# Optimization experiments

Hardware: AMD Instinct MI355X
Metric: run time of the kernel (lower is better)

Reference implementation:

```python
import jax, jax.numpy as jnp
import numpy as np

D_MODEL = 1024
NUM_HEADS = 16
HEAD_DIM = D_MODEL // NUM_HEADS
BATCH, SEQ = 4, 4096


def setup_inputs() -> dict:
    key = jax.random.key(0)
    ks = jax.random.split(key, 12)
    std = 0.02
    inp = {
        "query": jax.random.normal(ks[0], (BATCH, SEQ, D_MODEL), dtype=jnp.float32),
        "key": jax.random.normal(ks[1], (BATCH, SEQ, D_MODEL), dtype=jnp.float32),
        "value": jax.random.normal(ks[2], (BATCH, SEQ, D_MODEL), dtype=jnp.float32),
        "mask": jax.random.randint(ks[3], (BATCH, SEQ, 1, 1), 0, 2, dtype=jnp.int32),
        "Wq": jax.random.normal(ks[4], (D_MODEL, D_MODEL), dtype=jnp.float32) * std,
        "bq": jnp.zeros((D_MODEL,), dtype=jnp.float32),
        "Wk": jax.random.normal(ks[5], (D_MODEL, D_MODEL), dtype=jnp.float32) * std,
        "bk": jnp.zeros((D_MODEL,), dtype=jnp.float32),
        "Wv": jax.random.normal(ks[6], (D_MODEL, D_MODEL), dtype=jnp.float32) * std,
        "bv": jnp.zeros((D_MODEL,), dtype=jnp.float32),
        "Wo": jax.random.normal(ks[7], (D_MODEL, D_MODEL), dtype=jnp.float32) * std,
        "bo": jnp.zeros((D_MODEL,), dtype=jnp.float32),
    }
    return inp


def reference(query, key, value, mask, Wq, bq, Wk, bk, Wv, bv, Wo, bo):
    b = query.shape[0]
    # QKV projections (torch nn.Linear: x @ W.T + b)
    Q = query @ Wq.T + bq
    K = key @ Wk.T + bk
    V = value @ Wv.T + bv
    # [b, s, H, hd] -> [b, H, s, hd]
    Q = Q.reshape(b, -1, NUM_HEADS, HEAD_DIM).transpose(0, 2, 1, 3)
    K = K.reshape(b, -1, NUM_HEADS, HEAD_DIM).transpose(0, 2, 1, 3)
    V = V.reshape(b, -1, NUM_HEADS, HEAD_DIM).transpose(0, 2, 1, 3)
    # NOTE: faithful to the original's mislabeled einsum: tensors are [b,H,s,hd]
    # but labels treat axis1 as 'q' and axis2 as 'h', so energy is
    # [batch, seq, heads_q, heads_k] and softmax mixes over heads.
    energy = jnp.einsum('nqhd,nkhd->nhqk', Q, K)
    energy = jnp.where(mask == 0, jnp.float32(-1e20), energy)
    attention = jax.nn.softmax(energy / jnp.sqrt(jnp.float32(D_MODEL)), axis=3)
    # output labeled nqhd -> [b, heads, seq, hd]
    x = jnp.einsum('nhql,nlhd->nqhd', attention, V)
    x = x.transpose(0, 2, 1, 3).reshape(b, -1, D_MODEL)  # [b, s, d_model]
    return x @ Wo.T + bo
```

## Files before the change

kernel.cpp:

```cpp
#include <hip/hip_runtime.h>


typedef unsigned int u32;
typedef unsigned short u16;
typedef __attribute__((ext_vector_type(4))) float f32x4;
typedef __attribute__((ext_vector_type(8))) short bf16x8;

__device__ __forceinline__ void async_copy16(const void* g, void* l) {
  __builtin_amdgcn_global_load_lds(
      (const __attribute__((address_space(1))) void*)g,
      (__attribute__((address_space(3))) void*)l, 16, 0, 0);
}

__device__ __forceinline__ u32 pk_bf16(float a, float b) {
  u32 ua = (__builtin_bit_cast(u32, a) + 0x8000u) >> 16;
  u32 ub = (__builtin_bit_cast(u32, b) + 0x8000u) & 0xFFFF0000u;
  return ua | ub;
}
__device__ __forceinline__ float bflo(u32 u) { return __builtin_bit_cast(float, u << 16); }
__device__ __forceinline__ float bfhi(u32 u) { return __builtin_bit_cast(float, u & 0xFFFF0000u); }

struct F8 { float f[8]; };
__device__ __forceinline__ F8 unp8(uint4 u) {
  F8 r;
  r.f[0] = bflo(u.x); r.f[1] = bfhi(u.x);
  r.f[2] = bflo(u.y); r.f[3] = bfhi(u.y);
  r.f[4] = bflo(u.z); r.f[5] = bfhi(u.z);
  r.f[6] = bflo(u.w); r.f[7] = bfhi(u.w);
  return r;
}

__global__ void cvt_w4(const float* __restrict__ s0, const float* __restrict__ s1,
                       const float* __restrict__ s2, const float* __restrict__ s3,
                       u16* __restrict__ dst) {
  int z = blockIdx.y;
  const float* s = (z == 0) ? s0 : (z == 1) ? s1 : (z == 2) ? s2 : s3;
  u16* d = dst + (size_t)z * (1024 * 1024);
  int i = (blockIdx.x * 256 + threadIdx.x) * 4;
  float4 f = *(const float4*)(s + i);
  uint2 u;
  u.x = pk_bf16(f.x, f.y);
  u.y = pk_bf16(f.z, f.w);
  *(uint2*)(d + i) = u;
}

template <bool AF32, bool OUTBF>
__device__ __forceinline__ void gemm_tile(const void* __restrict__ Ap,
                                          const u16* __restrict__ Bp,
                                          const float* __restrict__ bias,
                                          void* __restrict__ Cp,
                                          int m0, int n0, u16* As, u16* Bs) {
  constexpr int KD = 1024;
  constexpr int ND = 1024;
  const int t = threadIdx.x;
  const int lane = t & 63, w = t >> 6;
  const int wr = (w >> 1) * 64, wc = (w & 1) * 64;
  const int lr = lane & 15, quad = lane >> 4;
  f32x4 acc[4][4] = {};

  for (int k0 = 0; k0 < KD; k0 += 32) {
    __syncthreads();
#pragma unroll
    for (int i = 0; i < 2; i++) {
      int c = i * 256 + t;
      int r = c >> 2, c8 = (c & 3) * 8;
      async_copy16(Bp + ((size_t)(n0 + r) * KD + k0 + c8), &Bs[c * 8]);
    }
    if constexpr (AF32) {
      const float* Af = (const float*)Ap;
      const int r = t >> 2, c8 = (t & 3) * 8;
      const float4* s0 = (const float4*)(Af + (size_t)(m0 + r) * KD + k0 + c8);
      const float4* s1 = (const float4*)(Af + (size_t)(m0 + 64 + r) * KD + k0 + c8);
      float4 f0 = s0[0], f1 = s0[1];
      float4 f2 = s1[0], f3 = s1[1];
      uint4 u0 = { pk_bf16(f0.x, f0.y), pk_bf16(f0.z, f0.w),
                   pk_bf16(f1.x, f1.y), pk_bf16(f1.z, f1.w) };
      uint4 u1 = { pk_bf16(f2.x, f2.y), pk_bf16(f2.z, f2.w),
                   pk_bf16(f3.x, f3.y), pk_bf16(f3.z, f3.w) };
      *(uint4*)&As[t * 8] = u0;
      *(uint4*)&As[(256 + t) * 8] = u1;
    } else {
      const u16* Ab = (const u16*)Ap;
#pragma unroll
      for (int i = 0; i < 2; i++) {
        int c = i * 256 + t;
        int r = c >> 2, c8 = (c & 3) * 8;
        async_copy16(Ab + ((size_t)(m0 + r) * KD + k0 + c8), &As[c * 8]);
      }
    }
    __syncthreads();

    bf16x8 af[4], bfr[4];
#pragma unroll
    for (int mi = 0; mi < 4; mi++)
      af[mi] = *(const bf16x8*)&As[(wr + mi * 16 + lr) * 32 + quad * 8];
#pragma unroll
    for (int ni = 0; ni < 4; ni++)
      bfr[ni] = *(const bf16x8*)&Bs[(wc + ni * 16 + lr) * 32 + quad * 8];
#pragma unroll
    for (int mi = 0; mi < 4; mi++)
#pragma unroll
      for (int ni = 0; ni < 4; ni++)
        acc[mi][ni] = __builtin_amdgcn_mfma_f32_16x16x32_bf16(af[mi], bfr[ni], acc[mi][ni], 0, 0, 0);
  }

#pragma unroll
  for (int ni = 0; ni < 4; ni++) {
    int col = n0 + wc + ni * 16 + lr;
    float bv = bias[col];
#pragma unroll
    for (int mi = 0; mi < 4; mi++) {
      int row = m0 + wr + mi * 16 + quad * 4;
#pragma unroll
      for (int r = 0; r < 4; r++) {
        float val = acc[mi][ni][r] + bv;
        if constexpr (OUTBF) {
          ((u16*)Cp)[(size_t)(row + r) * ND + col] =
              (u16)((__builtin_bit_cast(u32, val) + 0x8000u) >> 16);
        } else {
          ((float*)Cp)[(size_t)(row + r) * ND + col] = val;
        }
      }
    }
  }
}

__global__ __launch_bounds__(256) void gemm_qkv(
    const float* __restrict__ q, const float* __restrict__ k, const float* __restrict__ v,
    const u16* __restrict__ W, const float* __restrict__ bq, const float* __restrict__ bk,
    const float* __restrict__ bv, u16* __restrict__ out) {
  __shared__ alignas(16) u16 As[128 * 32];
  __shared__ alignas(16) u16 Bs[128 * 32];
  const int z = blockIdx.z;
  const float* A = (z == 0) ? q : (z == 1) ? k : v;
  const float* bias = (z == 0) ? bq : (z == 1) ? bk : bv;
  gemm_tile<true, true>(A, W + (size_t)z * 1048576, bias, out + (size_t)z * 16777216,
                        blockIdx.x * 128, blockIdx.y * 128, As, Bs);
}

__global__ __launch_bounds__(256) void gemm_o(
    const u16* __restrict__ X, const u16* __restrict__ W,
    const float* __restrict__ bias, float* __restrict__ C) {
  __shared__ alignas(16) u16 As[128 * 32];
  __shared__ alignas(16) u16 Bs[128 * 32];
  gemm_tile<false, false>(X, W, bias, C, blockIdx.x * 128, blockIdx.y * 128, As, Bs);
}

__global__ __launch_bounds__(256) void attn_mix(
    const u16* __restrict__ Q, const u16* __restrict__ K,
    const u16* __restrict__ V, const int* __restrict__ mask,
    u16* __restrict__ X) {
  __shared__ alignas(16) u16 qs[4][1024];
  __shared__ alignas(16) u16 ks[4][1024];
  __shared__ alignas(16) u16 vs[4][1024];

  const int w = threadIdx.x >> 6;
  const int lane = threadIdx.x & 63;
  const int p = blockIdx.x * 4 + w;
  const size_t base = (size_t)p * 1024;

  {
    const uint4* Qg = (const uint4*)(Q + base);
    const uint4* Kg = (const uint4*)(K + base);
    const uint4* Vg = (const uint4*)(V + base);
    uint4* ql = (uint4*)qs[w]; uint4* kl = (uint4*)ks[w]; uint4* vl = (uint4*)vs[w];
    ql[lane] = Qg[lane]; ql[64 + lane] = Qg[64 + lane];
    kl[lane] = Kg[lane]; kl[64 + lane] = Kg[64 + lane];
    vl[lane] = Vg[lane]; vl[64 + lane] = Vg[64 + lane];
  }
  const int mk = mask[p];

  const int qh = lane >> 2, g = lane & 3;
  float e0 = 0.f, e1 = 0.f, e2 = 0.f, e3 = 0.f;
  {
    const uint4* qr = (const uint4*)&qs[w][qh * 64];
    const uint4* k0r = (const uint4*)&ks[w][(g * 4 + 0) * 64];
    const uint4* k1r = (const uint4*)&ks[w][(g * 4 + 1) * 64];
    const uint4* k2r = (const uint4*)&ks[w][(g * 4 + 2) * 64];
    const uint4* k3r = (const uint4*)&ks[w][(g * 4 + 3) * 64];
#pragma unroll
    for (int c = 0; c < 8; c++) {
      F8 qf = unp8(qr[c]);
      F8 ka = unp8(k0r[c]), kb = unp8(k1r[c]), kc = unp8(k2r[c]), kd = unp8(k3r[c]);
#pragma unroll
      for (int j = 0; j < 8; j++) {
        e0 += qf.f[j] * ka.f[j];
        e1 += qf.f[j] * kb.f[j];
        e2 += qf.f[j] * kc.f[j];
        e3 += qf.f[j] * kd.f[j];
      }
    }
  }
  const float sc = mk ? 0.03125f : 0.0f;
  float v0 = e0 * sc, v1 = e1 * sc, v2 = e2 * sc, v3 = e3 * sc;
  float mx = fmaxf(fmaxf(v0, v1), fmaxf(v2, v3));
  mx = fmaxf(mx, __shfl_xor(mx, 1, 64));
  mx = fmaxf(mx, __shfl_xor(mx, 2, 64));
  float p0 = __expf(v0 - mx), p1 = __expf(v1 - mx), p2 = __expf(v2 - mx), p3 = __expf(v3 - mx);
  float s = p0 + p1 + p2 + p3;
  s += __shfl_xor(s, 1, 64);
  s += __shfl_xor(s, 2, 64);
  float inv = 1.0f / s;
  float a0 = p0 * inv, a1 = p1 * inv, a2 = p2 * inv, a3 = p3 * inv;

  const int c4 = g;
  float xa[16];
#pragma unroll
  for (int i = 0; i < 16; i++) xa[i] = 0.f;
#pragma unroll
  for (int g2 = 0; g2 < 4; g2++) {
    int src = (lane & ~3) | g2;
    float w0 = __shfl(a0, src, 64);
    float w1 = __shfl(a1, src, 64);
    float w2 = __shfl(a2, src, 64);
    float w3 = __shfl(a3, src, 64);
    const float wv[4] = { w0, w1, w2, w3 };
#pragma unroll
    for (int j4 = 0; j4 < 4; j4++) {
      int kh = g2 * 4 + j4;
      float wgt = wv[j4];
      F8 va = unp8(*(const uint4*)&vs[w][kh * 64 + c4 * 16]);
      F8 vb = unp8(*(const uint4*)&vs[w][kh * 64 + c4 * 16 + 8]);
#pragma unroll
      for (int j = 0; j < 8; j++) {
        xa[j] += wgt * va.f[j];
        xa[8 + j] += wgt * vb.f[j];
      }
    }
  }
  uint4 o0 = { pk_bf16(xa[0], xa[1]), pk_bf16(xa[2], xa[3]),
               pk_bf16(xa[4], xa[5]), pk_bf16(xa[6], xa[7]) };
  uint4 o1 = { pk_bf16(xa[8], xa[9]), pk_bf16(xa[10], xa[11]),
               pk_bf16(xa[12], xa[13]), pk_bf16(xa[14], xa[15]) };
  uint4* Xp = (uint4*)(X + base);
  Xp[lane * 2] = o0;
  Xp[lane * 2 + 1] = o1;
}

extern "C" void kernel_launch(void* const* d_in, const int* in_sizes, int n_in,
                              void* d_out, int out_size, void* d_ws, size_t ws_size,
                              hipStream_t stream) {
  const float* q    = (const float*)d_in[0];
  const float* k    = (const float*)d_in[1];
  const float* v    = (const float*)d_in[2];
  const int*   mask = (const int*)d_in[3];
  const float* Wq   = (const float*)d_in[4];
  const float* bq   = (const float*)d_in[5];
  const float* Wk   = (const float*)d_in[6];
  const float* bk   = (const float*)d_in[7];
  const float* Wv   = (const float*)d_in[8];
  const float* bv   = (const float*)d_in[9];
  const float* Wo   = (const float*)d_in[10];
  const float* bo   = (const float*)d_in[11];

  u16* wsb = (u16*)d_ws;
  u16* Wqkv = wsb;
  u16* Wob  = wsb + 3145728;
  u16* Qb   = wsb + 4194304;
  u16* Kb   = Qb + 16777216;
  u16* Vb   = Kb + 16777216;
  u16* Xb   = Vb + 16777216;

  cvt_w4<<<dim3(1024, 4), 256, 0, stream>>>(Wq, Wk, Wv, Wo, wsb);
  gemm_qkv<<<dim3(128, 8, 3), 256, 0, stream>>>(q, k, v, Wqkv, bq, bk, bv, Qb);
  attn_mix<<<4096, 256, 0, stream>>>(Qb, Kb, Vb, mask, Xb);
  gemm_o<<<dim3(128, 8), 256, 0, stream>>>(Xb, Wob, bo, (float*)d_out);
}
```

Before: 483.4 us.

## Pre-convert QKV inputs to bf16, remap GEMM tile order, pad attention LDS rows

When the workspace is large enough, a new kernel converts the fp32 query/key/value activations to bf16 before the QKV GEMM, so the GEMM streams half the bytes and skips per-tile conversion. The cost is an extra full pass over the inputs. Both GEMMs now use a linearized grid with a remapped block order that groups tiles sharing A rows, aiming at better L2 reuse. The attention kernel pads each 64-element head row in shared memory to 72 elements to reduce LDS bank conflicts.

```diff
diff --git a/kernel.cpp b/kernel.cpp
--- a/kernel.cpp
+++ b/kernel.cpp
@@ -36,6 +36,19 @@
   int z = blockIdx.y;
   const float* s = (z == 0) ? s0 : (z == 1) ? s1 : (z == 2) ? s2 : s3;
   u16* d = dst + (size_t)z * (1024 * 1024);
+  int i = (blockIdx.x * 256 + threadIdx.x) * 4;
+  float4 f = *(const float4*)(s + i);
+  uint2 u;
+  u.x = pk_bf16(f.x, f.y);
+  u.y = pk_bf16(f.z, f.w);
+  *(uint2*)(d + i) = u;
+}
+
+__global__ void cvt_in3(const float* __restrict__ s0, const float* __restrict__ s1,
+                        const float* __restrict__ s2, u16* __restrict__ dst) {
+  int z = blockIdx.y;
+  const float* s = (z == 0) ? s0 : (z == 1) ? s1 : s2;
+  u16* d = dst + (size_t)z * 16777216;
   int i = (blockIdx.x * 256 + threadIdx.x) * 4;
   float4 f = *(const float4*)(s + i);
   uint2 u;
@@ -125,17 +138,24 @@
   }
 }
 
+template <bool AF32>
 __global__ __launch_bounds__(256) void gemm_qkv(
-    const float* __restrict__ q, const float* __restrict__ k, const float* __restrict__ v,
-    const u16* __restrict__ W, const float* __restrict__ bq, const float* __restrict__ bk,
-    const float* __restrict__ bv, u16* __restrict__ out) {
+    const void* __restrict__ a0, const void* __restrict__ a1, const void* __restrict__ a2,
+    const u16* __restrict__ W, const float* __restrict__ b0, const float* __restrict__ b1,
+    const float* __restrict__ b2, u16* __restrict__ out) {
   __shared__ alignas(16) u16 As[128 * 32];
   __shared__ alignas(16) u16 Bs[128 * 32];
-  const int z = blockIdx.z;
-  const float* A = (z == 0) ? q : (z == 1) ? k : v;
-  const float* bias = (z == 0) ? bq : (z == 1) ? bk : bv;
-  gemm_tile<true, true>(A, W + (size_t)z * 1048576, bias, out + (size_t)z * 16777216,
-                        blockIdx.x * 128, blockIdx.y * 128, As, Bs);
+  const int lin = blockIdx.x;
+  const int c = lin & 7;
+  const int i = lin >> 3;
+  const int z = i >> 7;
+  const int r = i & 127;
+  const int m = c * 16 + (r >> 3);
+  const int n = r & 7;
+  const void* A = (z == 0) ? a0 : (z == 1) ? a1 : a2;
+  const float* bias = (z == 0) ? b0 : (z == 1) ? b1 : b2;
+  gemm_tile<AF32, true>(A, W + (size_t)z * 1048576, bias, out + (size_t)z * 16777216,
+                        m * 128, n * 128, As, Bs);
 }
 
 __global__ __launch_bounds__(256) void gemm_o(
@@ -143,16 +163,22 @@
     const float* __restrict__ bias, float* __restrict__ C) {
   __shared__ alignas(16) u16 As[128 * 32];
   __shared__ alignas(16) u16 Bs[128 * 32];
-  gemm_tile<false, false>(X, W, bias, C, blockIdx.x * 128, blockIdx.y * 128, As, Bs);
+  const int lin = blockIdx.x;
+  const int c = lin & 7;
+  const int i = lin >> 3;
+  const int m = c * 16 + (i >> 3);
+  const int n = i & 7;
+  gemm_tile<false, false>(X, W, bias, C, m * 128, n * 128, As, Bs);
 }
 
 __global__ __launch_bounds__(256) void attn_mix(
     const u16* __restrict__ Q, const u16* __restrict__ K,
     const u16* __restrict__ V, const int* __restrict__ mask,
     u16* __restrict__ X) {
-  __shared__ alignas(16) u16 qs[4][1024];
-  __shared__ alignas(16) u16 ks[4][1024];
-  __shared__ alignas(16) u16 vs[4][1024];
+  constexpr int RS = 72;
+  __shared__ alignas(16) u16 qs[4][16 * RS];
+  __shared__ alignas(16) u16 ks[4][16 * RS];
+  __shared__ alignas(16) u16 vs[4][16 * RS];
 
   const int w = threadIdx.x >> 6;
   const int lane = threadIdx.x & 63;
@@ -163,25 +189,32 @@
     const uint4* Qg = (const uint4*)(Q + base);
     const uint4* Kg = (const uint4*)(K + base);
     const uint4* Vg = (const uint4*)(V + base);
-    uint4* ql = (uint4*)qs[w]; uint4* kl = (uint4*)ks[w]; uint4* vl = (uint4*)vs[w];
-    ql[lane] = Qg[lane]; ql[64 + lane] = Qg[64 + lane];
-    kl[lane] = Kg[lane]; kl[64 + lane] = Kg[64 + lane];
-    vl[lane] = Vg[lane]; vl[64 + lane] = Vg[64 + lane];
+#pragma unroll
+    for (int h = 0; h < 2; h++) {
+      int j = h * 64 + lane;
+      int off = (j >> 3) * RS + (j & 7) * 8;
+      *(uint4*)&qs[w][off] = Qg[j];
+      *(uint4*)&ks[w][off] = Kg[j];
+      *(uint4*)&vs[w][off] = Vg[j];
+    }
   }
   const int mk = mask[p];
 
   const int qh = lane >> 2, g = lane & 3;
   float e0 = 0.f, e1 = 0.f, e2 = 0.f, e3 = 0.f;
   {
-    const uint4* qr = (const uint4*)&qs[w][qh * 64];
-    const uint4* k0r = (const uint4*)&ks[w][(g * 4 + 0) * 64];
-    const uint4* k1r = (const uint4*)&ks[w][(g * 4 + 1) * 64];
-    const uint4* k2r = (const uint4*)&ks[w][(g * 4 + 2) * 64];
-    const uint4* k3r = (const uint4*)&ks[w][(g * 4 + 3) * 64];
+    const u16* qr = &qs[w][qh * RS];
+    const u16* k0r = &ks[w][(g * 4 + 0) * RS];
+    const u16* k1r = &ks[w][(g * 4 + 1) * RS];
+    const u16* k2r = &ks[w][(g * 4 + 2) * RS];
+    const u16* k3r = &ks[w][(g * 4 + 3) * RS];
 #pragma unroll
     for (int c = 0; c < 8; c++) {
-      F8 qf = unp8(qr[c]);
-      F8 ka = unp8(k0r[c]), kb = unp8(k1r[c]), kc = unp8(k2r[c]), kd = unp8(k3r[c]);
+      F8 qf = unp8(*(const uint4*)&qr[c * 8]);
+      F8 ka = unp8(*(const uint4*)&k0r[c * 8]);
+      F8 kb = unp8(*(const uint4*)&k1r[c * 8]);
+      F8 kc = unp8(*(const uint4*)&k2r[c * 8]);
+      F8 kd = unp8(*(const uint4*)&k3r[c * 8]);
 #pragma unroll
       for (int j = 0; j < 8; j++) {
         e0 += qf.f[j] * ka.f[j];
@@ -203,7 +236,6 @@
   float inv = 1.0f / s;
   float a0 = p0 * inv, a1 = p1 * inv, a2 = p2 * inv, a3 = p3 * inv;
 
-  const int c4 = g;
   float xa[16];
 #pragma unroll
   for (int i = 0; i < 16; i++) xa[i] = 0.f;
@@ -219,8 +251,8 @@
     for (int j4 = 0; j4 < 4; j4++) {
       int kh = g2 * 4 + j4;
       float wgt = wv[j4];
-      F8 va = unp8(*(const uint4*)&vs[w][kh * 64 + c4 * 16]);
-      F8 vb = unp8(*(const uint4*)&vs[w][kh * 64 + c4 * 16 + 8]);
+      F8 va = unp8(*(const uint4*)&vs[w][kh * RS + g * 16]);
+      F8 vb = unp8(*(const uint4*)&vs[w][kh * RS + g * 16 + 8]);
 #pragma unroll
       for (int j = 0; j < 8; j++) {
         xa[j] += wgt * va.f[j];
@@ -254,15 +286,32 @@
   const float* bo   = (const float*)d_in[11];
 
   u16* wsb = (u16*)d_ws;
-  u16* Wqkv = wsb;
-  u16* Wob  = wsb + 3145728;
-  u16* Qb   = wsb + 4194304;
-  u16* Kb   = Qb + 16777216;
-  u16* Vb   = Kb + 16777216;
-  u16* Xb   = Vb + 16777216;
-
-  cvt_w4<<<dim3(1024, 4), 256, 0, stream>>>(Wq, Wk, Wv, Wo, wsb);
-  gemm_qkv<<<dim3(128, 8, 3), 256, 0, stream>>>(q, k, v, Wqkv, bq, bk, bv, Qb);
-  attn_mix<<<4096, 256, 0, stream>>>(Qb, Kb, Vb, mask, Xb);
-  gemm_o<<<dim3(128, 8), 256, 0, stream>>>(Xb, Wob, bo, (float*)d_out);
-}
+  const bool big = ws_size >= 209715200ull;
+
+  if (big) {
+    u16* Wqkv = wsb;
+    u16* Wob  = wsb + 3145728;
+    u16* qb   = wsb + 4194304;
+    u16* Qb   = wsb + 54525952;
+    u16* Kb   = Qb + 16777216;
+    u16* Vb   = Kb + 16777216;
+    u16* Xb   = qb;
+    cvt_w4<<<dim3(1024, 4), 256, 0, stream>>>(Wq, Wk, Wv, Wo, wsb);
+    cvt_in3<<<dim3(16384, 3), 256, 0, stream>>>(q, k, v, qb);
+    gemm_qkv<false><<<3072, 256, 0, stream>>>(qb, qb + 16777216, qb + 33554432,
+                                              Wqkv, bq, bk, bv, Qb);
+    attn_mix<<<4096, 256, 0, stream>>>(Qb, Kb, Vb, mask, Xb);
+    gemm_o<<<1024, 256, 0, stream>>>(Xb, Wob, bo, (float*)d_out);
+  } else {
+    u16* Wqkv = wsb;
+    u16* Wob  = wsb + 3145728;
+    u16* Qb   = wsb + 4194304;
+    u16* Kb   = Qb + 16777216;
+    u16* Vb   = Kb + 16777216;
+    u16* Xb   = Vb + 16777216;
+    cvt_w4<<<dim3(1024, 4), 256, 0, stream>>>(Wq, Wk, Wv, Wo, wsb);
+    gemm_qkv<true><<<3072, 256, 0, stream>>>(q, k, v, Wqkv, bq, bk, bv, Qb);
+    attn_mix<<<4096, 256, 0, stream>>>(Qb, Kb, Vb, mask, Xb);
+    gemm_o<<<1024, 256, 0, stream>>>(Xb, Wob, bo, (float*)d_out);
+  }
+}
```

After: 462.3 us. 1.05x faster.
